# Kernel optimization log

Hardware: AMD Instinct MI355X
Metric: run time of the kernel (lower is better)

Reference implementation:

```python
import jax, jax.numpy as jnp
import numpy as np

B, S, H, V, T = 32, 128, 256, 32000, 100


def setup_inputs() -> dict:
    key = jax.random.key(0)
    ks = jax.random.split(key, 16)
    s = 1.0 / np.sqrt(H)

    def u(k, shape):
        return jax.random.uniform(k, shape, jnp.float32, -s, s)

    return dict(
        enc_outputs=jax.random.normal(ks[0], (B, S, H), jnp.float32),
        enc_hidden=jax.random.normal(ks[1], (1, B, H), jnp.float32),
        target_tensor=jax.random.randint(ks[2], (B, T), 0, V),
        embedding=u(ks[3], (V, H)),
        Qw=u(ks[4], (H, H)), Qb=u(ks[5], (H,)),
        Kw=u(ks[6], (H, H)), Kb=u(ks[7], (H,)),
        Vw=u(ks[8], (1, H)), Vb=u(ks[9], (1,)),
        W_ih=u(ks[10], (3 * H, 2 * H)), W_hh=u(ks[11], (3 * H, H)),
        b_ih=u(ks[12], (3 * H,)), b_hh=u(ks[13], (3 * H,)),
        out_w=u(ks[14], (V, H)), out_b=u(ks[15], (V,)),
    )


def reference(enc_outputs, enc_hidden, target_tensor, embedding,
              Qw, Qb, Kw, Kb, Vw, Vb, W_ih, W_hh, b_ih, b_hh, out_w, out_b):
    # Teacher-forcing decode: dec_input starts at token 0, then target[:, i].
    Bv, Sv, Hd = enc_outputs.shape
    Tv = target_tensor.shape[1]
    # K(keys) is step-invariant: precompute once (same math as in-loop Linear).
    enc_k = enc_outputs @ Kw.T + Kb  # (B,S,H)
    tokens = jnp.concatenate(
        [jnp.zeros((Bv, 1), target_tensor.dtype), target_tensor[:, :-1]], axis=1)
    tokens_t = tokens.T  # (T,B)

    def step(h, tok):
        emb = embedding[tok]                                  # (B,H), dropout=eval noop
        q = h @ Qw.T + Qb                                     # query from hidden
        e = jnp.tanh(q[:, None, :] + enc_k)                   # (B,S,H) additive attn
        scores = jnp.einsum('bsh,h->bs', e, Vw[0]) + Vb[0]    # (B,S)
        w = jax.nn.softmax(scores, axis=-1)
        ctx = jnp.einsum('bs,bsh->bh', w, enc_outputs)        # bmm(weights, keys)
        x = jnp.concatenate([emb, ctx], axis=-1)              # (B,2H)
        gi = x @ W_ih.T + b_ih
        gh = h @ W_hh.T + b_hh
        r = jax.nn.sigmoid(gi[:, :Hd] + gh[:, :Hd])
        z = jax.nn.sigmoid(gi[:, Hd:2 * Hd] + gh[:, Hd:2 * Hd])
        n = jnp.tanh(gi[:, 2 * Hd:] + r * gh[:, 2 * Hd:])
        h_new = (1.0 - z) * n + z * h                         # torch GRU cell
        logits = h_new @ out_w.T + out_b                      # (B,V)
        return h_new, (logits, w)

    h_final, (logits, atts) = jax.lax.scan(step, enc_hidden[0], tokens_t)
    dec_outputs = jax.nn.log_softmax(jnp.transpose(logits, (1, 0, 2)), axis=-1)  # (B,T,V)
    atts = jnp.transpose(atts, (1, 0, 2))                     # (B,T,S)
    return dec_outputs, h_final[None], atts
```

## Files before the change

kernel.cpp:

```cpp
#include <hip/hip_runtime.h>
#include <hip/hip_bf16.h>

#define Bn 32
#define Sn 128
#define Hn 256
#define Vn 32000
#define Tn 100
#define GIn 768
#define AGENT __HIP_MEMORY_SCOPE_AGENT

typedef __attribute__((ext_vector_type(8))) short bf16x8;
typedef __attribute__((ext_vector_type(4))) float f32x4;

__device__ __forceinline__ float frcp(float x){ return __builtin_amdgcn_rcpf(x); }
__device__ __forceinline__ float ftanh(float x){ return 1.0f - 2.0f*frcp(__expf(2.0f*x)+1.0f); }
__device__ __forceinline__ float fsigm(float x){ return frcp(1.0f + __expf(-x)); }
__device__ __forceinline__ float b2f(unsigned short u){
  unsigned int v = ((unsigned int)u) << 16; return __builtin_bit_cast(float, v);
}
__device__ __forceinline__ unsigned short f2bu(float f){
  unsigned int u = __builtin_bit_cast(unsigned int, f);
  u += 0x7FFFu + ((u >> 16) & 1u);
  return (unsigned short)(u >> 16);
}
__device__ __forceinline__ void st_ag_u(unsigned int* p, unsigned int v){
  __hip_atomic_store(p, v, __ATOMIC_RELAXED, AGENT);
}
__device__ __forceinline__ unsigned int ld_ag_u(unsigned int* p){
  return __hip_atomic_load(p, __ATOMIC_RELAXED, AGENT);
}

__global__ __launch_bounds__(256) void k_tr(const float* __restrict__ in,
    float* __restrict__ out, int R, int C)
{
  __shared__ float tile[32][33];
  const int bx = blockIdx.x*32, by = blockIdx.y*32;
  const int tx = threadIdx.x & 31, ty = threadIdx.x >> 5;
  #pragma unroll
  for(int r = ty; r < 32; r += 8)
    if(by + r < R && bx + tx < C) tile[r][tx] = in[(size_t)(by + r)*C + bx + tx];
  __syncthreads();
  #pragma unroll
  for(int r = ty; r < 32; r += 8)
    if(bx + r < C && by + tx < R) out[(size_t)(bx + r)*R + by + tx] = tile[tx][r];
}

__global__ __launch_bounds__(256) void k_packW1R(const float* __restrict__ Qw,
    const float* __restrict__ Whh, unsigned short* __restrict__ W1R)
{
  const int tid = blockIdx.x*256 + threadIdx.x;
  const int lane = tid & 63;
  const int fragid = tid >> 6;
  const int tt = fragid % 5;
  const int kk = (fragid/5) % 8;
  const int w  = (fragid/40) % 8;
  const int hb = fragid/320;
  const int lr = lane & 15, lg = lane >> 4;
  const float* src;
  if(tt < 2){
    const int f = w*32 + tt*16 + lr;
    src = Qw + (size_t)f*Hn;
  } else {
    const int lf = w*48 + (tt-2)*16 + lr;
    const int g = lf >> 7, jj = lf & 127;
    src = Whh + (size_t)(g*256 + hb*128 + jj)*Hn;
  }
  const int col = kk*32 + lg*8;
  float4 v0 = *(const float4*)(src + col), v1 = *(const float4*)(src + col + 4);
  unsigned short* d = W1R + ((size_t)fragid*64 + lane)*8;
  d[0]=f2bu(v0.x); d[1]=f2bu(v0.y); d[2]=f2bu(v0.z); d[3]=f2bu(v0.w);
  d[4]=f2bu(v1.x); d[5]=f2bu(v1.y); d[6]=f2bu(v1.z); d[7]=f2bu(v1.w);
}

__global__ __launch_bounds__(256) void k_cvt(const float* __restrict__ src,
    __hip_bfloat16* __restrict__ dst, int n)
{
  int i = (blockIdx.x*256 + threadIdx.x)*4;
  if(i < n){
    float4 v = *(const float4*)(src + i);
    dst[i+0] = __float2bfloat16(v.x);
    dst[i+1] = __float2bfloat16(v.y);
    dst[i+2] = __float2bfloat16(v.z);
    dst[i+3] = __float2bfloat16(v.w);
  }
}

__global__ __launch_bounds__(256) void k_enc2(const float* __restrict__ enc_outputs,
    const float* __restrict__ KwT, const float* __restrict__ Kb,
    unsigned short* __restrict__ enc_kb16)
{
  const int r0 = blockIdx.x*16, j = threadIdx.x;
  __shared__ __align__(16) float encl[Hn][20];
  #pragma unroll
  for(int r = 0; r < 16; r++) encl[j][r] = enc_outputs[(size_t)(r0 + r)*Hn + j];
  __syncthreads();
  float acc[16];
  #pragma unroll
  for(int r = 0; r < 16; r++) acc[r] = Kb[j];
  for(int d = 0; d < Hn; d++){
    const float wv = KwT[(size_t)d*Hn + j];
    const float4 e0 = *(const float4*)&encl[d][0];
    const float4 e1 = *(const float4*)&encl[d][4];
    const float4 e2 = *(const float4*)&encl[d][8];
    const float4 e3 = *(const float4*)&encl[d][12];
    acc[0]+=e0.x*wv; acc[1]+=e0.y*wv; acc[2]+=e0.z*wv; acc[3]+=e0.w*wv;
    acc[4]+=e1.x*wv; acc[5]+=e1.y*wv; acc[6]+=e1.z*wv; acc[7]+=e1.w*wv;
    acc[8]+=e2.x*wv; acc[9]+=e2.y*wv; acc[10]+=e2.z*wv; acc[11]+=e2.w*wv;
    acc[12]+=e3.x*wv; acc[13]+=e3.y*wv; acc[14]+=e3.z*wv; acc[15]+=e3.w*wv;
  }
  #pragma unroll
  for(int r = 0; r < 16; r++) enc_kb16[(size_t)(r0 + r)*Hn + j] = f2bu(acc[r]);
}

__global__ __launch_bounds__(256) void k_packEk(const unsigned short* __restrict__ enc_kb16,
    unsigned short* __restrict__ ekP)
{
  const int tid = blockIdx.x*256 + threadIdx.x;
  const int b = tid >> 12;
  const int o = tid & 4095;
  const int g = o >> 6, l = o & 63;
  const int w = g >> 3, i = g & 7;
  const int s = w*16 + (l >> 2);
  const int e0 = i*32 + (l & 3)*8;
  const int4 v = *(const int4*)(enc_kb16 + ((size_t)(b*Sn + s))*Hn + e0);
  *(int4*)(ekP + (size_t)b*32768 + (size_t)o*8) = v;
}

__global__ __launch_bounds__(768) void k_encW2F(const float* __restrict__ enc_outputs,
    const float* __restrict__ W_ihT, unsigned short* __restrict__ encW2F)
{
  const int r0 = blockIdx.x*16, tid = threadIdx.x;
  __shared__ __align__(16) float encl[Hn][20];
  if(tid < Hn){
    #pragma unroll
    for(int r = 0; r < 16; r++) encl[tid][r] = enc_outputs[(size_t)(r0 + r)*Hn + tid];
  }
  __syncthreads();
  float acc[16];
  #pragma unroll
  for(int r = 0; r < 16; r++) acc[r] = 0.f;
  for(int d = 0; d < Hn; d++){
    const float wv = W_ihT[(size_t)(Hn + d)*GIn + tid];
    const float4 e0 = *(const float4*)&encl[d][0];
    const float4 e1 = *(const float4*)&encl[d][4];
    const float4 e2 = *(const float4*)&encl[d][8];
    const float4 e3 = *(const float4*)&encl[d][12];
    acc[0]+=e0.x*wv; acc[1]+=e0.y*wv; acc[2]+=e0.z*wv; acc[3]+=e0.w*wv;
    acc[4]+=e1.x*wv; acc[5]+=e1.y*wv; acc[6]+=e1.z*wv; acc[7]+=e1.w*wv;
    acc[8]+=e2.x*wv; acc[9]+=e2.y*wv; acc[10]+=e2.z*wv; acc[11]+=e2.w*wv;
    acc[12]+=e3.x*wv; acc[13]+=e3.y*wv; acc[14]+=e3.z*wv; acc[15]+=e3.w*wv;
  }
  const int g = tid >> 8, jj = tid & 255;
  const int hb = jj >> 7, jl = jj & 127;
  const int c = g*128 + jl;
  const int wvv = c/48, rem = c - wvv*48, tt = rem >> 4, lr = rem & 15;
  #pragma unroll
  for(int r = 0; r < 16; r++){
    const int bs = r0 + r;
    const int bb = bs >> 7, s = bs & 127;
    const int kk = s >> 5, lg = (s >> 3) & 3, e = s & 7;
    const int lane = lg*16 + lr;
    encW2F[(size_t)(bb*2 + hb)*49152 + (size_t)((wvv*12 + tt*4 + kk)*64 + lane)*8 + e]
        = f2bu(acc[r]);
  }
}

__global__ __launch_bounds__(768) void k_giemb2(const int* __restrict__ target,
    const float* __restrict__ embedding, const float* __restrict__ W_ihT,
    const float* __restrict__ b_ih, float* __restrict__ gi_emb)
{
  const int r0 = blockIdx.x*16, tid = threadIdx.x;
  __shared__ __align__(16) float embl[Hn][20];
  if(tid < Hn){
    #pragma unroll
    for(int r = 0; r < 16; r++){
      const int row = r0 + r;
      const int t = row >> 5, b = row & 31;
      const int tok = (t == 0) ? 0 : target[b*Tn + (t-1)];
      embl[tid][r] = embedding[(size_t)tok*Hn + tid];
    }
  }
  __syncthreads();
  float acc[16];
  #pragma unroll
  for(int r = 0; r < 16; r++) acc[r] = b_ih[tid];
  for(int d = 0; d < Hn; d++){
    const float wv = W_ihT[(size_t)d*GIn + tid];
    const float4 e0 = *(const float4*)&embl[d][0];
    const float4 e1 = *(const float4*)&embl[d][4];
    const float4 e2 = *(const float4*)&embl[d][8];
    const float4 e3 = *(const float4*)&embl[d][12];
    acc[0]+=e0.x*wv; acc[1]+=e0.y*wv; acc[2]+=e0.z*wv; acc[3]+=e0.w*wv;
    acc[4]+=e1.x*wv; acc[5]+=e1.y*wv; acc[6]+=e1.z*wv; acc[7]+=e1.w*wv;
    acc[8]+=e2.x*wv; acc[9]+=e2.y*wv; acc[10]+=e2.z*wv; acc[11]+=e2.w*wv;
    acc[12]+=e3.x*wv; acc[13]+=e3.y*wv; acc[14]+=e3.z*wv; acc[15]+=e3.w*wv;
  }
  #pragma unroll
  for(int r = 0; r < 16; r++) gi_emb[(size_t)(r0 + r)*GIn + tid] = acc[r];
}

__global__ __launch_bounds__(512, 2) void k_loop7(
    const float* __restrict__ enc_hidden,
    const unsigned short* __restrict__ ekP,
    const unsigned short* __restrict__ encW2F,
    const unsigned short* __restrict__ W1R,
    const float* __restrict__ Qb, const float* __restrict__ b_hh,
    const float* __restrict__ Vw, const float* __restrict__ Vb,
    const float* __restrict__ gi_emb,
    __hip_bfloat16* __restrict__ h_all,
    float* __restrict__ atts_out,
    float* __restrict__ hfin_out,
    unsigned int* hbuf,
    unsigned int* hflag)
{
  const int bid = blockIdx.x;
  const int hb = (bid >> 3) & 1;
  const int p  = (bid & 7) | ((bid >> 4) << 3);
  const int b = p;
  const int tid = threadIdx.x;
  const int lane = tid & 63, wv = tid >> 6;
  const int lr = lane & 15, lg = lane >> 4;

  __shared__ __align__(16) unsigned short ew_l[49152];
  __shared__ __align__(16) float h_sh[128];
  __shared__ __align__(16) short h_b16[Hn];
  __shared__ __align__(16) float qgh_sh[1024];
  __shared__ __align__(16) float vw_sh[Hn];
  __shared__ __align__(16) float sc_sh[Sn];
  __shared__ __align__(16) unsigned short wb_l[Sn];
  __shared__ __align__(16) float gic_l[384];

  {
    const unsigned short* src = encW2F + (size_t)(b*2 + hb)*49152;
    #pragma unroll
    for(int c = 0; c < 12; c++){
      const int idx = (c*512 + tid)*8;
      *(int4*)(ew_l + idx) = *(const int4*)(src + idx);
    }
  }
  bf16x8 ekr[8];
  {
    const unsigned short* esrc = ekP + (size_t)b*32768;
    #pragma unroll
    for(int i = 0; i < 8; i++)
      ekr[i] = *(const bf16x8*)(esrc + (size_t)((wv*8 + i)*64 + lane)*8);
  }
  bf16x8 w1f[40];
  {
    const unsigned short* wsrc = W1R + (((size_t)(hb*8 + wv)*40)*64 + lane)*8;
    #pragma unroll
    for(int f = 0; f < 40; f++) w1f[f] = *(const bf16x8*)(wsrc + (size_t)f*512);
  }
  float bias_r[5]; int idx_r[5];
  #pragma unroll
  for(int tt = 0; tt < 2; tt++){
    const int f = wv*32 + tt*16 + lr;
    bias_r[tt] = Qb[f]; idx_r[tt] = f;
  }
  #pragma unroll
  for(int tt = 2; tt < 5; tt++){
    const int lf = wv*48 + (tt-2)*16 + lr;
    const int g = lf >> 7, jj = lf & 127;
    bias_r[tt] = b_hh[g*256 + hb*128 + jj];
    idx_r[tt]  = 256 + g*256 + hb*128 + jj;
  }
  if(tid < Hn){
    vw_sh[tid] = Vw[tid];
    h_b16[tid] = (short)f2bu(enc_hidden[b*Hn + tid]);
  }
  if(tid < 128) h_sh[tid] = enc_hidden[b*Hn + hb*128 + tid];
  __syncthreads();
  const float vb0 = Vb[0];
  const int g2 = tid & 3;

  for(int t = 0; t < Tn; t++){
    const int par = t & 1;
    {
      f32x4 acc[5];
      #pragma unroll
      for(int tt = 0; tt < 5; tt++) acc[tt] = (f32x4){0.f,0.f,0.f,0.f};
      #pragma unroll
      for(int kk = 0; kk < 8; kk++){
        bf16x8 a = *(const bf16x8*)(h_b16 + kk*32 + lg*8);
        #pragma unroll
        for(int tt = 0; tt < 5; tt++)
          acc[tt] = __builtin_amdgcn_mfma_f32_16x16x32_bf16(a, w1f[kk*5 + tt], acc[tt], 0, 0, 0);
      }
      if(lane < 16){
        #pragma unroll
        for(int tt = 0; tt < 5; tt++)
          qgh_sh[idx_r[tt]] = acc[tt][0] + bias_r[tt];
      }
    }
    __syncthreads();

    {
      float pacc = 0.f;
      #pragma unroll
      for(int i = 0; i < 8; i++){
        const bf16x8 e8 = ekr[i];
        const int kb = i*32 + g2*8;
        #pragma unroll
        for(int j = 0; j < 8; j++){
          float ev = b2f((unsigned short)e8[j]);
          pacc = fmaf(vw_sh[kb + j], ftanh(qgh_sh[kb + j] + ev), pacc);
        }
      }
      pacc += __shfl_xor(pacc, 1); pacc += __shfl_xor(pacc, 2);
      if(g2 == 0) sc_sh[tid >> 2] = pacc + vb0;
    }
    __syncthreads();

    if(tid < 64){
      float v0 = sc_sh[tid], v1 = sc_sh[tid + 64];
      float m = fmaxf(v0, v1);
      #pragma unroll
      for(int off = 1; off < 64; off <<= 1) m = fmaxf(m, __shfl_xor(m, off));
      float e0 = __expf(v0 - m), e1 = __expf(v1 - m);
      float sm = e0 + e1;
      #pragma unroll
      for(int off = 1; off < 64; off <<= 1) sm += __shfl_xor(sm, off);
      float inv = frcp(sm);
      float w0 = e0*inv, w1 = e1*inv;
      wb_l[tid] = f2bu(w0); wb_l[tid + 64] = f2bu(w1);
      if(hb == 0){
        float* ao = atts_out + ((size_t)b*Tn + t)*Sn;
        ao[tid] = w0; ao[tid + 64] = w1;
      }
    }
    float ge0 = 0.f, ge1 = 0.f, ge2 = 0.f;
    if(tid < 128){
      const float* ge = gi_emb + ((size_t)t*Bn + b)*GIn + hb*128 + tid;
      ge0 = ge[0]; ge1 = ge[256]; ge2 = ge[512];
    }
    __syncthreads();

    {
      bf16x8 wfrag[4];
      #pragma unroll
      for(int kk = 0; kk < 4; kk++)
        wfrag[kk] = *(const bf16x8*)(wb_l + kk*32 + lg*8);
      #pragma unroll
      for(int tt = 0; tt < 3; tt++){
        f32x4 a3 = (f32x4){0.f,0.f,0.f,0.f};
        #pragma unroll
        for(int kk = 0; kk < 4; kk++){
          bf16x8 bfr = *(const bf16x8*)(ew_l + (size_t)((wv*12 + tt*4 + kk)*64 + lane)*8);
          a3 = __builtin_amdgcn_mfma_f32_16x16x32_bf16(wfrag[kk], bfr, a3, 0, 0, 0);
        }
        if(lane < 16) gic_l[wv*48 + tt*16 + lane] = a3[0];
      }
    }
    __syncthreads();

    if(tid < 128){
      float gr = ge0 + gic_l[tid];
      float gz = ge1 + gic_l[128 + tid];
      float gn = ge2 + gic_l[256 + tid];
      const int jg = hb*128 + tid;
      float r = fsigm(gr + qgh_sh[256 + jg]);
      float z = fsigm(gz + qgh_sh[512 + jg]);
      float n = ftanh(gn + r*qgh_sh[768 + jg]);
      float hn2 = (1.0f - z)*n + z*h_sh[tid];
      h_sh[tid] = hn2;
      const unsigned short hb16 = f2bu(hn2);
      h_b16[jg] = (short)hb16;
      h_all[((size_t)t*Bn + b)*Hn + jg] = __float2bfloat16(hn2);
      if(t == Tn-1) hfin_out[b*Hn + jg] = hn2;
      if(t < Tn-1){
        float hnx = __shfl_down(hn2, 1);
        if(!(tid & 1)){
          unsigned int u = (unsigned int)hb16 | ((unsigned int)f2bu(hnx) << 16);
          st_ag_u(&hbuf[((size_t)(par*32 + p)*2 + hb)*64 + (tid >> 1)], u);
        }
      }
    }
    __syncthreads();

    if(t < Tn-1){
      if(tid == 0)
        __hip_atomic_store(&hflag[p*2 + hb], (unsigned)(t + 1), __ATOMIC_RELEASE, AGENT);
      if(tid < 64){
        long cnt = 0;
        while(__hip_atomic_load(&hflag[p*2 + (hb^1)], __ATOMIC_ACQUIRE, AGENT) < (unsigned)(t + 1)
              && ++cnt < 10000000L){}
        unsigned int u = ld_ag_u(&hbuf[((size_t)(par*32 + p)*2 + (hb^1))*64 + tid]);
        ((unsigned int*)h_b16)[(hb^1)*64 + tid] = u;
      }
      __syncthreads();
    }
  }
}

__global__ __launch_bounds__(512, 2) void k_logits2(
    const short* __restrict__ h_all, const short* __restrict__ w_bf,
    const float* __restrict__ out_b,
    float* __restrict__ pmax, float* __restrict__ psum,
    const float* __restrict__ lse, float* __restrict__ dec_out,
    int pass)
{
  const int tid = threadIdx.x;
  const int wave = tid >> 6, lane = tid & 63;
  const int lr = lane & 15, lg = lane >> 4;
  const int wm = wave >> 2, wn = wave & 3;
  const int n0 = blockIdx.x*256 + wn*64;
  const int m0 = blockIdx.y*256 + wm*128;
  f32x4 acc[8][4];
  #pragma unroll
  for(int mt = 0; mt < 8; mt++)
    #pragma unroll
    for(int nt = 0; nt < 4; nt++) acc[mt][nt] = (f32x4){0.f,0.f,0.f,0.f};
  #pragma unroll
  for(int kk = 0; kk < 8; kk++){
    bf16x8 am[8], bn[4];
    #pragma unroll
    for(int mt = 0; mt < 8; mt++){
      int row = m0 + mt*16 + lr; row = row < 3200 ? row : 3199;
      am[mt] = *(const bf16x8*)(h_all + (size_t)row*Hn + kk*32 + lg*8);
    }
    #pragma unroll
    for(int nt = 0; nt < 4; nt++)
      bn[nt] = *(const bf16x8*)(w_bf + (size_t)(n0 + nt*16 + lr)*Hn + kk*32 + lg*8);
    #pragma unroll
    for(int mt = 0; mt < 8; mt++)
      #pragma unroll
      for(int nt = 0; nt < 4; nt++)
        acc[mt][nt] = __builtin_amdgcn_mfma_f32_16x16x32_bf16(am[mt], bn[nt], acc[mt][nt], 0, 0, 0);
  }
  float bias[4];
  #pragma unroll
  for(int nt = 0; nt < 4; nt++) bias[nt] = out_b[n0 + nt*16 + lr];

  if(pass == 0){
    __shared__ float pm_l[256][4];
    __shared__ float ps_l[256][4];
    #pragma unroll
    for(int mt = 0; mt < 8; mt++){
      #pragma unroll
      for(int i = 0; i < 4; i++){
        float v0 = acc[mt][0][i] + bias[0], v1 = acc[mt][1][i] + bias[1];
        float v2 = acc[mt][2][i] + bias[2], v3 = acc[mt][3][i] + bias[3];
        float m = fmaxf(fmaxf(v0, v1), fmaxf(v2, v3));
        m = fmaxf(m, __shfl_xor(m, 1)); m = fmaxf(m, __shfl_xor(m, 2));
        m = fmaxf(m, __shfl_xor(m, 4)); m = fmaxf(m, __shfl_xor(m, 8));
        float s = __expf(v0 - m) + __expf(v1 - m) + __expf(v2 - m) + __expf(v3 - m);
        s += __shfl_xor(s, 1); s += __shfl_xor(s, 2);
        s += __shfl_xor(s, 4); s += __shfl_xor(s, 8);
        if(lr == 0){
          const int rl = wm*128 + mt*16 + lg*4 + i;
          pm_l[rl][wn] = m; ps_l[rl][wn] = s;
        }
      }
    }
    __syncthreads();
    if(tid < 256){
      const int rg = blockIdx.y*256 + tid;
      if(rg < 3200){
        float m = fmaxf(fmaxf(pm_l[tid][0], pm_l[tid][1]), fmaxf(pm_l[tid][2], pm_l[tid][3]));
        float s = ps_l[tid][0]*__expf(pm_l[tid][0] - m) + ps_l[tid][1]*__expf(pm_l[tid][1] - m)
                + ps_l[tid][2]*__expf(pm_l[tid][2] - m) + ps_l[tid][3]*__expf(pm_l[tid][3] - m);
        pmax[(size_t)blockIdx.x*3200 + rg] = m;
        psum[(size_t)blockIdx.x*3200 + rg] = s;
      }
    }
  } else {
    #pragma unroll
    for(int mt = 0; mt < 8; mt++){
      #pragma unroll
      for(int i = 0; i < 4; i++){
        const int rg = blockIdx.y*256 + wm*128 + mt*16 + lg*4 + i;
        if(rg < 3200){
          const float l = lse[rg];
          const int bb = rg & 31, tt2 = rg >> 5;
          float* dst = dec_out + (size_t)bb*((size_t)Tn*Vn) + (size_t)tt2*Vn + n0;
          dst[ 0 + lr] = acc[mt][0][i] + bias[0] - l;
          dst[16 + lr] = acc[mt][1][i] + bias[1] - l;
          dst[32 + lr] = acc[mt][2][i] + bias[2] - l;
          dst[48 + lr] = acc[mt][3][i] + bias[3] - l;
        }
      }
    }
  }
}

__global__ __launch_bounds__(256) void k_lse(const float* __restrict__ pmax,
    const float* __restrict__ psum, float* __restrict__ lse)
{
  const int row = blockIdx.x*256 + threadIdx.x;
  if(row >= Tn*Bn) return;
  float m = -3.0e38f;
  for(int c = 0; c < 125; c++) m = fmaxf(m, pmax[(size_t)c*3200 + row]);
  float s = 0.f;
  for(int c = 0; c < 125; c++)
    s += psum[(size_t)c*3200 + row] * __expf(pmax[(size_t)c*3200 + row] - m);
  lse[row] = m + __logf(s);
}

extern "C" void kernel_launch(void* const* d_in, const int* in_sizes, int n_in,
                              void* d_out, int out_size, void* d_ws, size_t ws_size,
                              hipStream_t stream)
{
  const float* enc_outputs = (const float*)d_in[0];
  const float* enc_hidden  = (const float*)d_in[1];
  const int*   target      = (const int*)d_in[2];
  const float* embedding   = (const float*)d_in[3];
  const float* Qw   = (const float*)d_in[4];
  const float* Qb   = (const float*)d_in[5];
  const float* Kw   = (const float*)d_in[6];
  const float* Kb   = (const float*)d_in[7];
  const float* Vw   = (const float*)d_in[8];
  const float* Vb   = (const float*)d_in[9];
  const float* W_ih = (const float*)d_in[10];
  const float* W_hh = (const float*)d_in[11];
  const float* b_ih = (const float*)d_in[12];
  const float* b_hh = (const float*)d_in[13];
  const float* out_w = (const float*)d_in[14];
  const float* out_b = (const float*)d_in[15];

  float* dec  = (float*)d_out;
  float* hfin = dec + (size_t)Bn*Tn*Vn;
  float* atts = hfin + Bn*Hn;

  unsigned short* enc_kb16 = (unsigned short*)(dec);
  unsigned short* ekP      = (unsigned short*)(dec + 524288);
  unsigned short* encW2F   = (unsigned short*)(dec + 1048576);
  float* gi_emb = dec + 2621440;
  float* W_ihT  = dec + 5079040;
  float* KwT    = dec + 5472256;
  float* pmax   = dec + 5537792;
  float* psum   = dec + 5937792;
  unsigned short* W1R = (unsigned short*)(dec + 6337792);
  unsigned int* hbuf  = (unsigned int*)(dec + 6501632);
  unsigned int* hflag = (unsigned int*)(dec + 6509824);

  float* wsf = (float*)d_ws;
  float* lse = wsf;
  __hip_bfloat16* h_all = (__hip_bfloat16*)(wsf + 3200);
  __hip_bfloat16* w_bf  = h_all + (size_t)Tn*Bn*Hn;

  k_tr     <<<dim3(8, 8),   dim3(256), 0, stream>>>(Kw, KwT, 256, 256);
  k_tr     <<<dim3(16, 24), dim3(256), 0, stream>>>(W_ih, W_ihT, 768, 512);
  k_packW1R<<<dim3(160),    dim3(256), 0, stream>>>(Qw, W_hh, W1R);
  k_cvt    <<<dim3((Vn*Hn)/1024), dim3(256), 0, stream>>>(out_w, w_bf, Vn*Hn);
  k_enc2   <<<dim3(256), dim3(256), 0, stream>>>(enc_outputs, KwT, Kb, enc_kb16);
  k_packEk <<<dim3(512), dim3(256), 0, stream>>>(enc_kb16, ekP);
  k_encW2F <<<dim3(256), dim3(768), 0, stream>>>(enc_outputs, W_ihT, encW2F);
  k_giemb2 <<<dim3(200), dim3(768), 0, stream>>>(target, embedding, W_ihT, b_ih, gi_emb);

  hipMemsetAsync((void*)hflag, 0, 64*sizeof(unsigned int), stream);

  k_loop7 <<<dim3(64), dim3(512), 0, stream>>>(enc_hidden, ekP, encW2F, W1R,
            Qb, b_hh, Vw, Vb, gi_emb, h_all, atts, hfin, hbuf, hflag);

  k_logits2<<<dim3(125, 13), dim3(512), 0, stream>>>(
            (const short*)h_all, (const short*)w_bf, out_b,
            pmax, psum, (const float*)nullptr, (float*)nullptr, 0);
  k_lse    <<<dim3(13), dim3(256), 0, stream>>>(pmax, psum, lse);
  k_logits2<<<dim3(125, 13), dim3(512), 0, stream>>>(
            (const short*)h_all, (const short*)w_bf, out_b,
            (float*)nullptr, (float*)nullptr, lse, dec, 1);
}
```

Measured before the change: 1.400 ms.

## Overlap recurrent half-state exchange with local MFMA and retile logits GEMM via LDS

The recurrent loop now keeps only its own half of the hidden state in LDS. It starts the Q/W_hh MFMAs on that half before spinning on the partner block's flag, then reads the partner half straight from global hbuf. This hides part of the cross-block handshake latency and moves the attention and h_all stores off the critical path. The logits GEMM becomes 128x128 tiles with double-buffered LDS staging in 256-thread blocks, which doubles the number of partial max/sum columns the LSE pass must reduce. The new flag protocol (t+2 values, initial publish) changes synchronisation subtly and carries some correctness risk.

After: 1.842 ms. 1.32x slower.

```diff
diff --git a/kernel.cpp b/kernel.cpp
--- a/kernel.cpp
+++ b/kernel.cpp
@@ -199,7 +199,7 @@
   for(int r = 0; r < 16; r++) gi_emb[(size_t)(r0 + r)*GIn + tid] = acc[r];
 }
 
-__global__ __launch_bounds__(512, 2) void k_loop7(
+__global__ __launch_bounds__(512, 2) void k_loop8(
     const float* __restrict__ enc_hidden,
     const unsigned short* __restrict__ ekP,
     const unsigned short* __restrict__ encW2F,
@@ -223,7 +223,7 @@
 
   __shared__ __align__(16) unsigned short ew_l[49152];
   __shared__ __align__(16) float h_sh[128];
-  __shared__ __align__(16) short h_b16[Hn];
+  __shared__ __align__(16) unsigned short hown_l[128];
   __shared__ __align__(16) float qgh_sh[1024];
   __shared__ __align__(16) float vw_sh[Hn];
   __shared__ __align__(16) float sc_sh[Sn];
@@ -264,35 +264,73 @@
     bias_r[tt] = b_hh[g*256 + hb*128 + jj];
     idx_r[tt]  = 256 + g*256 + hb*128 + jj;
   }
-  if(tid < Hn){
-    vw_sh[tid] = Vw[tid];
-    h_b16[tid] = (short)f2bu(enc_hidden[b*Hn + tid]);
-  }
-  if(tid < 128) h_sh[tid] = enc_hidden[b*Hn + hb*128 + tid];
+  if(tid < Hn) vw_sh[tid] = Vw[tid];
+  if(tid < 128){
+    float hv = enc_hidden[b*Hn + hb*128 + tid];
+    h_sh[tid] = hv; hown_l[tid] = f2bu(hv);
+  }
+  if(tid < 64){
+    float h0 = enc_hidden[b*Hn + hb*128 + tid*2];
+    float h1 = enc_hidden[b*Hn + hb*128 + tid*2 + 1];
+    unsigned int u = (unsigned int)f2bu(h0) | ((unsigned int)f2bu(h1) << 16);
+    st_ag_u(&hbuf[((size_t)(0*32 + p)*2 + hb)*64 + tid], u);
+  }
   __syncthreads();
+  if(tid == 0)
+    __hip_atomic_store(&hflag[p*2 + hb], 1u, __ATOMIC_RELEASE, AGENT);
+
   const float vb0 = Vb[0];
   const int g2 = tid & 3;
 
   for(int t = 0; t < Tn; t++){
     const int par = t & 1;
+    f32x4 acc[5];
+    #pragma unroll
+    for(int tt = 0; tt < 5; tt++) acc[tt] = (f32x4){0.f,0.f,0.f,0.f};
+    #pragma unroll
+    for(int kkl = 0; kkl < 4; kkl++){
+      bf16x8 a = *(const bf16x8*)(hown_l + kkl*32 + lg*8);
+      const int kf = (hb*4 + kkl)*5;
+      #pragma unroll
+      for(int tt = 0; tt < 5; tt++)
+        acc[tt] = __builtin_amdgcn_mfma_f32_16x16x32_bf16(a, w1f[kf + tt], acc[tt], 0, 0, 0);
+    }
     {
-      f32x4 acc[5];
-      #pragma unroll
-      for(int tt = 0; tt < 5; tt++) acc[tt] = (f32x4){0.f,0.f,0.f,0.f};
-      #pragma unroll
-      for(int kk = 0; kk < 8; kk++){
-        bf16x8 a = *(const bf16x8*)(h_b16 + kk*32 + lg*8);
+      long cnt = 0;
+      while(__hip_atomic_load(&hflag[p*2 + (hb^1)], __ATOMIC_ACQUIRE, AGENT) < (unsigned)(t + 1)
+            && ++cnt < 10000000L){}
+    }
+    {
+      unsigned int* hsrc = hbuf + ((size_t)(par*32 + p)*2 + (hb^1))*64;
+      #pragma unroll
+      for(int kkl = 0; kkl < 4; kkl++){
+        unsigned int u0 = ld_ag_u(hsrc + kkl*16 + lg*4);
+        unsigned int u1 = ld_ag_u(hsrc + kkl*16 + lg*4 + 1);
+        unsigned int u2 = ld_ag_u(hsrc + kkl*16 + lg*4 + 2);
+        unsigned int u3 = ld_ag_u(hsrc + kkl*16 + lg*4 + 3);
+        bf16x8 a;
+        a[0]=(short)(u0&0xFFFF); a[1]=(short)(u0>>16);
+        a[2]=(short)(u1&0xFFFF); a[3]=(short)(u1>>16);
+        a[4]=(short)(u2&0xFFFF); a[5]=(short)(u2>>16);
+        a[6]=(short)(u3&0xFFFF); a[7]=(short)(u3>>16);
+        const int kf = ((1-hb)*4 + kkl)*5;
         #pragma unroll
         for(int tt = 0; tt < 5; tt++)
-          acc[tt] = __builtin_amdgcn_mfma_f32_16x16x32_bf16(a, w1f[kk*5 + tt], acc[tt], 0, 0, 0);
+          acc[tt] = __builtin_amdgcn_mfma_f32_16x16x32_bf16(a, w1f[kf + tt], acc[tt], 0, 0, 0);
       }
-      if(lane < 16){
-        #pragma unroll
-        for(int tt = 0; tt < 5; tt++)
-          qgh_sh[idx_r[tt]] = acc[tt][0] + bias_r[tt];
-      }
+    }
+    if(lane < 16){
+      #pragma unroll
+      for(int tt = 0; tt < 5; tt++)
+        qgh_sh[idx_r[tt]] = acc[tt][0] + bias_r[tt];
     }
     __syncthreads();
+
+    float ge0 = 0.f, ge1 = 0.f, ge2 = 0.f;
+    if(tid < 128){
+      const float* ge = gi_emb + ((size_t)t*Bn + b)*GIn + hb*128 + tid;
+      ge0 = ge[0]; ge1 = ge[256]; ge2 = ge[512];
+    }
 
     {
       float pacc = 0.f;
@@ -311,6 +349,7 @@
     }
     __syncthreads();
 
+    float w0 = 0.f, w1 = 0.f;
     if(tid < 64){
       float v0 = sc_sh[tid], v1 = sc_sh[tid + 64];
       float m = fmaxf(v0, v1);
@@ -321,19 +360,15 @@
       #pragma unroll
       for(int off = 1; off < 64; off <<= 1) sm += __shfl_xor(sm, off);
       float inv = frcp(sm);
-      float w0 = e0*inv, w1 = e1*inv;
+      w0 = e0*inv; w1 = e1*inv;
       wb_l[tid] = f2bu(w0); wb_l[tid + 64] = f2bu(w1);
-      if(hb == 0){
-        float* ao = atts_out + ((size_t)b*Tn + t)*Sn;
-        ao[tid] = w0; ao[tid + 64] = w1;
-      }
-    }
-    float ge0 = 0.f, ge1 = 0.f, ge2 = 0.f;
-    if(tid < 128){
-      const float* ge = gi_emb + ((size_t)t*Bn + b)*GIn + hb*128 + tid;
-      ge0 = ge[0]; ge1 = ge[256]; ge2 = ge[512];
     }
     __syncthreads();
+
+    if(tid < 64 && hb == 0){
+      float* ao = atts_out + ((size_t)b*Tn + t)*Sn;
+      ao[tid] = w0; ao[tid + 64] = w1;
+    }
 
     {
       bf16x8 wfrag[4];
@@ -353,6 +388,7 @@
     }
     __syncthreads();
 
+    float hn2 = 0.f;
     if(tid < 128){
       float gr = ge0 + gic_l[tid];
       float gz = ge1 + gic_l[128 + tid];
@@ -361,81 +397,109 @@
       float r = fsigm(gr + qgh_sh[256 + jg]);
       float z = fsigm(gz + qgh_sh[512 + jg]);
       float n = ftanh(gn + r*qgh_sh[768 + jg]);
-      float hn2 = (1.0f - z)*n + z*h_sh[tid];
+      hn2 = (1.0f - z)*n + z*h_sh[tid];
       h_sh[tid] = hn2;
       const unsigned short hb16 = f2bu(hn2);
-      h_b16[jg] = (short)hb16;
-      h_all[((size_t)t*Bn + b)*Hn + jg] = __float2bfloat16(hn2);
-      if(t == Tn-1) hfin_out[b*Hn + jg] = hn2;
+      hown_l[tid] = hb16;
       if(t < Tn-1){
         float hnx = __shfl_down(hn2, 1);
         if(!(tid & 1)){
           unsigned int u = (unsigned int)hb16 | ((unsigned int)f2bu(hnx) << 16);
-          st_ag_u(&hbuf[((size_t)(par*32 + p)*2 + hb)*64 + (tid >> 1)], u);
+          st_ag_u(&hbuf[((size_t)(((t+1)&1)*32 + p)*2 + hb)*64 + (tid >> 1)], u);
         }
       }
     }
     __syncthreads();
 
-    if(t < Tn-1){
-      if(tid == 0)
-        __hip_atomic_store(&hflag[p*2 + hb], (unsigned)(t + 1), __ATOMIC_RELEASE, AGENT);
-      if(tid < 64){
-        long cnt = 0;
-        while(__hip_atomic_load(&hflag[p*2 + (hb^1)], __ATOMIC_ACQUIRE, AGENT) < (unsigned)(t + 1)
-              && ++cnt < 10000000L){}
-        unsigned int u = ld_ag_u(&hbuf[((size_t)(par*32 + p)*2 + (hb^1))*64 + tid]);
-        ((unsigned int*)h_b16)[(hb^1)*64 + tid] = u;
-      }
-      __syncthreads();
-    }
-  }
-}
-
-__global__ __launch_bounds__(512, 2) void k_logits2(
-    const short* __restrict__ h_all, const short* __restrict__ w_bf,
+    if(tid == 0 && t < Tn-1)
+      __hip_atomic_store(&hflag[p*2 + hb], (unsigned)(t + 2), __ATOMIC_RELEASE, AGENT);
+    if(tid < 128){
+      const int jg = hb*128 + tid;
+      h_all[((size_t)t*Bn + b)*Hn + jg] = __float2bfloat16(hn2);
+      if(t == Tn-1) hfin_out[b*Hn + jg] = hn2;
+    }
+  }
+}
+
+__global__ __launch_bounds__(256, 2) void k_lg3(
+    const unsigned short* __restrict__ h_all, const unsigned short* __restrict__ w_bf,
     const float* __restrict__ out_b,
     float* __restrict__ pmax, float* __restrict__ psum,
     const float* __restrict__ lse, float* __restrict__ dec_out,
     int pass)
 {
   const int tid = threadIdx.x;
-  const int wave = tid >> 6, lane = tid & 63;
+  const int lane = tid & 63, w = tid >> 6;
   const int lr = lane & 15, lg = lane >> 4;
-  const int wm = wave >> 2, wn = wave & 3;
-  const int n0 = blockIdx.x*256 + wn*64;
-  const int m0 = blockIdx.y*256 + wm*128;
-  f32x4 acc[8][4];
-  #pragma unroll
-  for(int mt = 0; mt < 8; mt++)
+  const int wm = w >> 1, wn = w & 1;
+  const int n0 = blockIdx.x*128;
+  const int m0 = blockIdx.y*128;
+  __shared__ __align__(16) unsigned short As[2][128][72];
+  __shared__ __align__(16) unsigned short Bs[2][128][72];
+  const int srow = tid >> 2, scol = (tid & 3)*16;
+
+  f32x4 acc[4][4];
+  #pragma unroll
+  for(int mt = 0; mt < 4; mt++)
     #pragma unroll
     for(int nt = 0; nt < 4; nt++) acc[mt][nt] = (f32x4){0.f,0.f,0.f,0.f};
-  #pragma unroll
-  for(int kk = 0; kk < 8; kk++){
-    bf16x8 am[8], bn[4];
-    #pragma unroll
-    for(int mt = 0; mt < 8; mt++){
-      int row = m0 + mt*16 + lr; row = row < 3200 ? row : 3199;
-      am[mt] = *(const bf16x8*)(h_all + (size_t)row*Hn + kk*32 + lg*8);
-    }
+
+  auto stage = [&](int buf, int ks){
+    #pragma unroll
+    for(int i = 0; i < 2; i++){
+      const int r = i*64 + srow;
+      const size_t ga = (size_t)(m0 + r)*Hn + ks*64 + scol;
+      const size_t gb = (size_t)(n0 + r)*Hn + ks*64 + scol;
+      int4 a0 = *(const int4*)(h_all + ga);
+      int4 a1 = *(const int4*)(h_all + ga + 8);
+      int4 b0 = *(const int4*)(w_bf + gb);
+      int4 b1 = *(const int4*)(w_bf + gb + 8);
+      *(int4*)(&As[buf][r][scol])     = a0;
+      *(int4*)(&As[buf][r][scol + 8]) = a1;
+      *(int4*)(&Bs[buf][r][scol])     = b0;
+      *(int4*)(&Bs[buf][r][scol + 8]) = b1;
+    }
+  };
+  auto compute = [&](int buf){
+    bf16x8 am[4][2], bn[4][2];
+    #pragma unroll
+    for(int mt = 0; mt < 4; mt++)
+      #pragma unroll
+      for(int kk = 0; kk < 2; kk++)
+        am[mt][kk] = *(const bf16x8*)(&As[buf][wm*64 + mt*16 + lr][kk*32 + lg*8]);
     #pragma unroll
     for(int nt = 0; nt < 4; nt++)
-      bn[nt] = *(const bf16x8*)(w_bf + (size_t)(n0 + nt*16 + lr)*Hn + kk*32 + lg*8);
-    #pragma unroll
-    for(int mt = 0; mt < 8; mt++)
-      #pragma unroll
-      for(int nt = 0; nt < 4; nt++)
-        acc[mt][nt] = __builtin_amdgcn_mfma_f32_16x16x32_bf16(am[mt], bn[nt], acc[mt][nt], 0, 0, 0);
-  }
+      #pragma unroll
+      for(int kk = 0; kk < 2; kk++)
+        bn[nt][kk] = *(const bf16x8*)(&Bs[buf][wn*64 + nt*16 + lr][kk*32 + lg*8]);
+    #pragma unroll
+    for(int kk = 0; kk < 2; kk++)
+      #pragma unroll
+      for(int mt = 0; mt < 4; mt++)
+        #pragma unroll
+        for(int nt = 0; nt < 4; nt++)
+          acc[mt][nt] = __builtin_amdgcn_mfma_f32_16x16x32_bf16(am[mt][kk], bn[nt][kk], acc[mt][nt], 0, 0, 0);
+  };
+
+  stage(0, 0);
+  __syncthreads();
+  #pragma unroll
+  for(int ks = 0; ks < 4; ks++){
+    const int buf = ks & 1;
+    if(ks < 3) stage(buf^1, ks+1);
+    compute(buf);
+    __syncthreads();
+  }
+
   float bias[4];
   #pragma unroll
-  for(int nt = 0; nt < 4; nt++) bias[nt] = out_b[n0 + nt*16 + lr];
+  for(int nt = 0; nt < 4; nt++) bias[nt] = out_b[n0 + wn*64 + nt*16 + lr];
 
   if(pass == 0){
-    __shared__ float pm_l[256][4];
-    __shared__ float ps_l[256][4];
-    #pragma unroll
-    for(int mt = 0; mt < 8; mt++){
+    __shared__ float pm_l[128][2];
+    __shared__ float ps_l[128][2];
+    #pragma unroll
+    for(int mt = 0; mt < 4; mt++){
       #pragma unroll
       for(int i = 0; i < 4; i++){
         float v0 = acc[mt][0][i] + bias[0], v1 = acc[mt][1][i] + bias[1];
@@ -447,37 +511,31 @@
         s += __shfl_xor(s, 1); s += __shfl_xor(s, 2);
         s += __shfl_xor(s, 4); s += __shfl_xor(s, 8);
         if(lr == 0){
-          const int rl = wm*128 + mt*16 + lg*4 + i;
+          const int rl = wm*64 + mt*16 + lg*4 + i;
           pm_l[rl][wn] = m; ps_l[rl][wn] = s;
         }
       }
     }
     __syncthreads();
-    if(tid < 256){
-      const int rg = blockIdx.y*256 + tid;
-      if(rg < 3200){
-        float m = fmaxf(fmaxf(pm_l[tid][0], pm_l[tid][1]), fmaxf(pm_l[tid][2], pm_l[tid][3]));
-        float s = ps_l[tid][0]*__expf(pm_l[tid][0] - m) + ps_l[tid][1]*__expf(pm_l[tid][1] - m)
-                + ps_l[tid][2]*__expf(pm_l[tid][2] - m) + ps_l[tid][3]*__expf(pm_l[tid][3] - m);
-        pmax[(size_t)blockIdx.x*3200 + rg] = m;
-        psum[(size_t)blockIdx.x*3200 + rg] = s;
-      }
+    if(tid < 128){
+      float m = fmaxf(pm_l[tid][0], pm_l[tid][1]);
+      float s = ps_l[tid][0]*__expf(pm_l[tid][0] - m) + ps_l[tid][1]*__expf(pm_l[tid][1] - m);
+      pmax[(size_t)blockIdx.x*3200 + m0 + tid] = m;
+      psum[(size_t)blockIdx.x*3200 + m0 + tid] = s;
     }
   } else {
     #pragma unroll
-    for(int mt = 0; mt < 8; mt++){
+    for(int mt = 0; mt < 4; mt++){
       #pragma unroll
       for(int i = 0; i < 4; i++){
-        const int rg = blockIdx.y*256 + wm*128 + mt*16 + lg*4 + i;
-        if(rg < 3200){
-          const float l = lse[rg];
-          const int bb = rg & 31, tt2 = rg >> 5;
-          float* dst = dec_out + (size_t)bb*((size_t)Tn*Vn) + (size_t)tt2*Vn + n0;
-          dst[ 0 + lr] = acc[mt][0][i] + bias[0] - l;
-          dst[16 + lr] = acc[mt][1][i] + bias[1] - l;
-          dst[32 + lr] = acc[mt][2][i] + bias[2] - l;
-          dst[48 + lr] = acc[mt][3][i] + bias[3] - l;
-        }
+        const int rg = m0 + wm*64 + mt*16 + lg*4 + i;
+        const float l = lse[rg];
+        const int bb = rg & 31, tt2 = rg >> 5;
+        float* dst = dec_out + (size_t)bb*((size_t)Tn*Vn) + (size_t)tt2*Vn + n0 + wn*64;
+        dst[ 0 + lr] = acc[mt][0][i] + bias[0] - l;
+        dst[16 + lr] = acc[mt][1][i] + bias[1] - l;
+        dst[32 + lr] = acc[mt][2][i] + bias[2] - l;
+        dst[48 + lr] = acc[mt][3][i] + bias[3] - l;
       }
     }
   }
@@ -489,9 +547,9 @@
   const int row = blockIdx.x*256 + threadIdx.x;
   if(row >= Tn*Bn) return;
   float m = -3.0e38f;
-  for(int c = 0; c < 125; c++) m = fmaxf(m, pmax[(size_t)c*3200 + row]);
+  for(int c = 0; c < 250; c++) m = fmaxf(m, pmax[(size_t)c*3200 + row]);
   float s = 0.f;
-  for(int c = 0; c < 125; c++)
+  for(int c = 0; c < 250; c++)
     s += psum[(size_t)c*3200 + row] * __expf(pmax[(size_t)c*3200 + row] - m);
   lse[row] = m + __logf(s);
 }
@@ -528,10 +586,10 @@
   float* W_ihT  = dec + 5079040;
   float* KwT    = dec + 5472256;
   float* pmax   = dec + 5537792;
-  float* psum   = dec + 5937792;
-  unsigned short* W1R = (unsigned short*)(dec + 6337792);
-  unsigned int* hbuf  = (unsigned int*)(dec + 6501632);
-  unsigned int* hflag = (unsigned int*)(dec + 6509824);
+  float* psum   = dec + 6337792;
+  unsigned short* W1R = (unsigned short*)(dec + 7137792);
+  unsigned int* hbuf  = (unsigned int*)(dec + 7301632);
+  unsigned int* hflag = (unsigned int*)(dec + 7309824);
 
   float* wsf = (float*)d_ws;
   float* lse = wsf;
@@ -549,14 +607,14 @@
 
   hipMemsetAsync((void*)hflag, 0, 64*sizeof(unsigned int), stream);
 
-  k_loop7 <<<dim3(64), dim3(512), 0, stream>>>(enc_hidden, ekP, encW2F, W1R,
+  k_loop8 <<<dim3(64), dim3(512), 0, stream>>>(enc_hidden, ekP, encW2F, W1R,
             Qb, b_hh, Vw, Vb, gi_emb, h_all, atts, hfin, hbuf, hflag);
 
-  k_logits2<<<dim3(125, 13), dim3(512), 0, stream>>>(
-            (const short*)h_all, (const short*)w_bf, out_b,
+  k_lg3   <<<dim3(250, 25), dim3(256), 0, stream>>>(
+            (const unsigned short*)h_all, (const unsigned short*)w_bf, out_b,
             pmax, psum, (const float*)nullptr, (float*)nullptr, 0);
-  k_lse    <<<dim3(13), dim3(256), 0, stream>>>(pmax, psum, lse);
-  k_logits2<<<dim3(125, 13), dim3(512), 0, stream>>>(
-            (const short*)h_all, (const short*)w_bf, out_b,
+  k_lse   <<<dim3(13), dim3(256), 0, stream>>>(pmax, psum, lse);
+  k_lg3   <<<dim3(250, 25), dim3(256), 0, stream>>>(
+            (const unsigned short*)h_all, (const unsigned short*)w_bf, out_b,
             (float*)nullptr, (float*)nullptr, lse, dec, 1);
 }
```
